# Optimization experiments

Hardware: AMD Instinct MI355X
Metric: run time of the kernel (lower is better)

The kernel has to match this reference:

```python
import jax, jax.numpy as jnp
import numpy as np

D_MODEL = 1024
D_HEAD = 128
BATCH = 4
SEQ = 4096


def setup_inputs() -> dict:
    key = jax.random.key(0)
    ks = jax.random.split(key, 7)
    s = 1.0 / np.sqrt(D_MODEL)
    return {
        "x": jax.random.normal(ks[0], (BATCH, SEQ, D_MODEL), dtype=jnp.float32),
        "Wq": jax.random.normal(ks[1], (D_MODEL, D_HEAD), dtype=jnp.float32) * s,
        "bq": jax.random.normal(ks[2], (D_HEAD,), dtype=jnp.float32) * 0.02,
        "Wk": jax.random.normal(ks[3], (D_MODEL, D_HEAD), dtype=jnp.float32) * s,
        "bk": jax.random.normal(ks[4], (D_HEAD,), dtype=jnp.float32) * 0.02,
        "Wv": jax.random.normal(ks[5], (D_MODEL, D_HEAD), dtype=jnp.float32) * s,
        "bv": jax.random.normal(ks[6], (D_HEAD,), dtype=jnp.float32) * 0.02,
    }


def reference(x, Wq, bq, Wk, bk, Wv, bv):
    # Single-head causal self-attention (intended math of MaskedAttention).
    # x: [B, S, D_MODEL]; projections to [B, S, D_HEAD].
    q = x @ Wq + bq
    k = x @ Wk + bk
    v = x @ Wv + bv
    scale = 1.0 / jnp.sqrt(jnp.asarray(D_HEAD, dtype=x.dtype))
    scores = jnp.einsum("bsd,btd->bst", q, k) * scale  # [B, S, S]
    # additive causal mask: -inf strictly above the diagonal
    s_len = scores.shape[-1]
    causal = jnp.tril(jnp.ones((s_len, s_len), dtype=bool))
    scores = jnp.where(causal[None, :, :], scores, jnp.asarray(-jnp.inf, dtype=scores.dtype))
    attn = jax.nn.softmax(scores, axis=-1)
    return jnp.einsum("bst,btd->bsd", attn, v)  # [B, S, D_HEAD]
```

## Files before the change

kernel.cpp:

```cpp
#include <hip/hip_runtime.h>
#include <stdint.h>
#include <stddef.h>

#define SEQ 4096
#define DM 1024
#define DH 128
#define NB 4
#define SPLITS 4

typedef __attribute__((ext_vector_type(8))) short bf16x8;
typedef __attribute__((ext_vector_type(4))) float f32x4;

__device__ __forceinline__ unsigned short f2bf(float f) {
    union { float f; uint32_t u; } v; v.f = f;
    uint32_t u = v.u + 0x7FFF + ((v.u >> 16) & 1);
    return (unsigned short)(u >> 16);
}

__device__ __forceinline__ uint32_t cvt_pk_bf16(float lo, float hi) {
    uint32_t r;
    asm("v_cvt_pk_bf16_f32 %0, %1, %2" : "=v"(r) : "v"(lo), "v"(hi));
    return r;
}

__device__ __forceinline__ void gload_lds16(const void* g, void* l) {
    __builtin_amdgcn_global_load_lds(
        (const __attribute__((address_space(1))) void*)g,
        (__attribute__((address_space(3))) void*)l, 16, 0, 0);
}

__global__ __launch_bounds__(256) void prep_kernel(
    const float* __restrict__ Wq, const float* __restrict__ Wk,
    const float* __restrict__ Wv, unsigned short* __restrict__ Wt)
{
    int idx = blockIdx.x * 256 + threadIdx.x;
    int n = idx >> 10, k = idx & 1023;
    int p = n >> 7, c = n & 127;
    const float* W = (p == 0) ? Wq : (p == 1) ? Wk : Wv;
    float v = W[k * DH + c];
    if (p == 0) v *= 0.08838834764831845f;
    Wt[idx] = f2bf(v);
}

__global__ __launch_bounds__(512) void proj_kernel(
    const float* __restrict__ x,
    const unsigned short* __restrict__ Wt,
    const float* __restrict__ bq, const float* __restrict__ bk,
    const float* __restrict__ bv,
    unsigned short* __restrict__ qb, unsigned short* __restrict__ kb,
    unsigned short* __restrict__ vt)
{
    __shared__ unsigned short A_lds[2][64 * 72];
    __shared__ unsigned short B_lds[2][384 * 64];
    const int tid = threadIdx.x;
    const int lane = tid & 63, w = tid >> 6;
    const int wm = w >> 2, wn = w & 3;
    const int q15 = lane & 15, g = lane >> 4;
    const int mt = blockIdx.x;

    const int arow = tid >> 3, aseg = tid & 7;

    f32x4 acc[2][6];
    #pragma unroll
    for (int mi = 0; mi < 2; ++mi)
        #pragma unroll
        for (int ni = 0; ni < 6; ++ni) acc[mi][ni] = (f32x4){0.f, 0.f, 0.f, 0.f};

    const float* asrc = x + (size_t)(mt * 64 + arow) * DM + aseg * 8;

    #pragma unroll
    for (int t = 0; t < 6; ++t) {
        int brow = t * 64 + arow;
        int bl = aseg ^ (brow & 7);
        gload_lds16(Wt + (size_t)brow * DM + bl * 8,
                    (char*)&B_lds[0][0] + t * 8192 + tid * 16);
    }
    {
        f32x4 lo4 = *(const f32x4*)asrc;
        f32x4 hi4 = *(const f32x4*)(asrc + 4);
        uint32_t* ad = (uint32_t*)&A_lds[0][arow * 72 + aseg * 8];
        ad[0] = cvt_pk_bf16(lo4[0], lo4[1]);
        ad[1] = cvt_pk_bf16(lo4[2], lo4[3]);
        ad[2] = cvt_pk_bf16(hi4[0], hi4[1]);
        ad[3] = cvt_pk_bf16(hi4[2], hi4[3]);
    }
    __syncthreads();

    int cur = 0;
    for (int kt = 0; kt < 16; ++kt) {
        f32x4 nlo, nhi;
        if (kt < 15) {
            #pragma unroll
            for (int t = 0; t < 6; ++t) {
                int brow = t * 64 + arow;
                int bl = aseg ^ (brow & 7);
                gload_lds16(Wt + (size_t)brow * DM + (kt + 1) * 64 + bl * 8,
                            (char*)&B_lds[cur ^ 1][0] + t * 8192 + tid * 16);
            }
            nlo = *(const f32x4*)(asrc + (kt + 1) * 64);
            nhi = *(const f32x4*)(asrc + (kt + 1) * 64 + 4);
        }
        #pragma unroll
        for (int kk = 0; kk < 2; ++kk) {
            bf16x8 af[2], bfr[6];
            #pragma unroll
            for (int mi = 0; mi < 2; ++mi)
                af[mi] = *(const bf16x8*)&A_lds[cur][(wm * 32 + mi * 16 + q15) * 72 + (kk * 4 + g) * 8];
            #pragma unroll
            for (int ni = 0; ni < 6; ++ni)
                bfr[ni] = *(const bf16x8*)&B_lds[cur][(wn * 96 + ni * 16 + q15) * 64 + ((kk * 4 + g) ^ (q15 & 7)) * 8];
            #pragma unroll
            for (int mi = 0; mi < 2; ++mi)
                #pragma unroll
                for (int ni = 0; ni < 6; ++ni)
                    acc[mi][ni] = __builtin_amdgcn_mfma_f32_16x16x32_bf16(
                        af[mi], bfr[ni], acc[mi][ni], 0, 0, 0);
        }
        if (kt < 15) {
            uint32_t* ad = (uint32_t*)&A_lds[cur ^ 1][arow * 72 + aseg * 8];
            ad[0] = cvt_pk_bf16(nlo[0], nlo[1]);
            ad[1] = cvt_pk_bf16(nlo[2], nlo[3]);
            ad[2] = cvt_pk_bf16(nhi[0], nhi[1]);
            ad[3] = cvt_pk_bf16(nhi[2], nhi[3]);
        }
        __syncthreads();
        cur ^= 1;
    }

    #pragma unroll
    for (int ni = 0; ni < 6; ++ni) {
        int n = wn * 96 + ni * 16 + q15;
        int p = n >> 7, c = n & 127;
        const float* bias = (p == 0) ? bq : (p == 1) ? bk : bv;
        float bval = bias[c] * ((p == 0) ? 0.08838834764831845f : 1.0f);
        #pragma unroll
        for (int mi = 0; mi < 2; ++mi) {
            int m0 = mt * 64 + wm * 32 + mi * 16 + g * 4;
            #pragma unroll
            for (int r = 0; r < 4; ++r) {
                unsigned short h = f2bf(acc[mi][ni][r] + bval);
                int m = m0 + r;
                if (p == 0) qb[(size_t)m * DH + c] = h;
                else if (p == 1) kb[(size_t)m * DH + c] = h;
                else vt[(size_t)((m >> 12) * 128 + c) * SEQ + (m & 4095)] = h;
            }
        }
    }
}

__global__ __launch_bounds__(512) void attn_kernel(
    const unsigned short* __restrict__ qb,
    const unsigned short* __restrict__ kb,
    const unsigned short* __restrict__ vt,
    float* __restrict__ po,
    float* __restrict__ pm, float* __restrict__ pl)
{
    __shared__ unsigned short K_lds[64 * 128];
    __shared__ unsigned short V_lds[128 * 64];
    __shared__ unsigned short P_lds[8 * 1024];
    const int tid = threadIdx.x;
    const int w = tid >> 6;
    const int lane = tid & 63;
    const int q15 = lane & 15, g = lane >> 4;
    const int xcd = blockIdx.x & 7, slot = blockIdx.x >> 3;
    const int b = xcd >> 1;
    const int j = 31 - (slot >> 1);
    const int s = (slot & 1) * 2 + (xcd & 1);
    const int n = 2 * j + 2;
    const int lo = (n * s) >> 2, hi = (n * (s + 1)) >> 2;
    if (lo >= hi) return;
    const int qbase = j * 128;
    const int wq0 = qbase + w * 16;
    const int qglob = wq0 + q15;

    bf16x8 qf[4];
    const unsigned short* qrow = qb + (size_t)(b * SEQ + qglob) * DH;
    #pragma unroll
    for (int kk = 0; kk < 4; ++kk) qf[kk] = *(const bf16x8*)(qrow + kk * 32 + g * 8);

    f32x4 o[8];
    #pragma unroll
    for (int f = 0; f < 8; ++f) o[f] = (f32x4){0.f, 0.f, 0.f, 0.f};
    float m_run = -60.0f, l_run = 0.f;

    const unsigned short* Kb = kb + (size_t)b * SEQ * DH;
    const unsigned short* Vb = vt + (size_t)b * 128 * SEQ;
    unsigned short* Pw = &P_lds[w * 1024];

    for (int kt = lo; kt < hi; ++kt) {
        {
            const unsigned short* Ksrc = Kb + (size_t)kt * 64 * DH;
            const unsigned short* Vsrc = Vb + kt * 64;
            #pragma unroll
            for (int i = 0; i < 2; ++i) {
                int krow = i * 32 + w * 4 + (lane >> 4);
                int kseg = (lane & 15) ^ (krow & 7);
                gload_lds16(Ksrc + (size_t)krow * DH + kseg * 8,
                            (char*)K_lds + i * 8192 + w * 1024);
                int vrow = i * 64 + w * 8 + (lane >> 3);
                int vseg = (lane & 7) ^ (vrow & 7);
                gload_lds16(Vsrc + (size_t)vrow * SEQ + vseg * 8,
                            (char*)V_lds + i * 8192 + w * 1024);
            }
        }
        __syncthreads();
        f32x4 sf[4];
        __builtin_amdgcn_s_setprio(1);
        #pragma unroll
        for (int mt2 = 0; mt2 < 4; ++mt2) {
            f32x4 sa = (f32x4){0.f, 0.f, 0.f, 0.f};
            #pragma unroll
            for (int kk = 0; kk < 4; ++kk) {
                int seg = (kk * 4 + g) ^ (q15 & 7);
                bf16x8 kf = *(const bf16x8*)&K_lds[(mt2 * 16 + q15) * 128 + seg * 8];
                sa = __builtin_amdgcn_mfma_f32_16x16x32_bf16(kf, qf[kk], sa, 0, 0, 0);
            }
            sf[mt2] = sa;
        }
        __builtin_amdgcn_s_setprio(0);
        float tmax = -__builtin_inff();
        if (kt * 64 + 63 > wq0) {
            #pragma unroll
            for (int mt2 = 0; mt2 < 4; ++mt2)
                #pragma unroll
                for (int r = 0; r < 4; ++r) {
                    int kglob = kt * 64 + mt2 * 16 + g * 4 + r;
                    float v = (kglob <= qglob) ? sf[mt2][r] : -__builtin_inff();
                    sf[mt2][r] = v;
                    tmax = fmaxf(tmax, v);
                }
        } else {
            #pragma unroll
            for (int mt2 = 0; mt2 < 4; ++mt2)
                #pragma unroll
                for (int r = 0; r < 4; ++r) tmax = fmaxf(tmax, sf[mt2][r]);
        }
        tmax = fmaxf(tmax, __shfl_xor(tmax, 16));
        tmax = fmaxf(tmax, __shfl_xor(tmax, 32));
        if (!__all((tmax - m_run) <= 8.0f)) {
            float m_new = fmaxf(m_run, tmax);
            float c = __expf(m_run - m_new);
            float cr[4];
            #pragma unroll
            for (int r = 0; r < 4; ++r) cr[r] = __shfl(c, g * 4 + r);
            #pragma unroll
            for (int f = 0; f < 8; ++f)
                #pragma unroll
                for (int r = 0; r < 4; ++r) o[f][r] *= cr[r];
            l_run *= c;
            m_run = m_new;
        }
        float rsum = 0.f;
        #pragma unroll
        for (int mt2 = 0; mt2 < 4; ++mt2)
            #pragma unroll
            for (int r = 0; r < 4; ++r) {
                float p = __expf(sf[mt2][r] - m_run);
                sf[mt2][r] = p;
                rsum += p;
            }
        rsum += __shfl_xor(rsum, 16);
        rsum += __shfl_xor(rsum, 32);
        l_run += rsum;
        #pragma unroll
        for (int mt2 = 0; mt2 < 4; ++mt2) {
            uint32_t p01 = cvt_pk_bf16(sf[mt2][0], sf[mt2][1]);
            uint32_t p23 = cvt_pk_bf16(sf[mt2][2], sf[mt2][3]);
            uint32_t* pd = (uint32_t*)(Pw + ((mt2 * 2 + (g >> 1)) * 16 + q15) * 8 + (g & 1) * 4);
            pd[0] = p01;
            pd[1] = p23;
        }
        asm volatile("s_waitcnt lgkmcnt(0)" ::: "memory");
        bf16x8 pf[2];
        #pragma unroll
        for (int kk2 = 0; kk2 < 2; ++kk2)
            pf[kk2] = *(const bf16x8*)&Pw[((kk2 * 4 + g) * 16 + q15) * 8];
        __builtin_amdgcn_s_setprio(1);
        #pragma unroll
        for (int f = 0; f < 8; ++f) {
            #pragma unroll
            for (int kk2 = 0; kk2 < 2; ++kk2) {
                int seg = (kk2 * 4 + g) ^ (q15 & 7);
                bf16x8 vf = *(const bf16x8*)&V_lds[(f * 16 + q15) * 64 + seg * 8];
                o[f] = __builtin_amdgcn_mfma_f32_16x16x32_bf16(pf[kk2], vf, o[f], 0, 0, 0);
            }
        }
        __builtin_amdgcn_s_setprio(0);
        __syncthreads();
    }
    float* pob = po + ((size_t)(s * NB + b) * SEQ + wq0) * DH;
    #pragma unroll
    for (int f = 0; f < 8; ++f)
        #pragma unroll
        for (int r = 0; r < 4; ++r)
            pob[(size_t)(g * 4 + r) * DH + f * 16 + q15] = o[f][r];
    if (g == 0) {
        size_t sidx = (size_t)(s * NB + b) * SEQ + wq0 + q15;
        pm[sidx] = m_run;
        pl[sidx] = l_run;
    }
}

__global__ __launch_bounds__(256) void reduce_kernel(
    const float* __restrict__ po, const float* __restrict__ pm,
    const float* __restrict__ pl, float* __restrict__ out)
{
    int r = blockIdx.x * 8 + (threadIdx.x >> 5);
    int d0 = (threadIdx.x & 31) * 4;
    int b = r >> 12, q = r & 4095;
    int n = 2 * (q >> 7) + 2;
    float ms[SPLITS];
    float M = -__builtin_inff();
    #pragma unroll
    for (int s = 0; s < SPLITS; ++s) {
        int lo = (n * s) >> 2, hi = (n * (s + 1)) >> 2;
        if (hi > lo) {
            ms[s] = pm[(size_t)(s * NB + b) * SEQ + q];
            M = fmaxf(M, ms[s]);
        } else ms[s] = -__builtin_inff();
    }
    float L = 0.f;
    f32x4 acc = (f32x4){0.f, 0.f, 0.f, 0.f};
    #pragma unroll
    for (int s = 0; s < SPLITS; ++s) {
        int lo = (n * s) >> 2, hi = (n * (s + 1)) >> 2;
        if (hi > lo) {
            float wgt = __expf(ms[s] - M);
            L += wgt * pl[(size_t)(s * NB + b) * SEQ + q];
            f32x4 p = *(const f32x4*)&po[((size_t)(s * NB + b) * SEQ + q) * DH + d0];
            acc += wgt * p;
        }
    }
    float inv = 1.0f / L;
    *(f32x4*)&out[((size_t)(b * SEQ) + q) * DH + d0] = acc * inv;
}

extern "C" void kernel_launch(void* const* d_in, const int* in_sizes, int n_in,
                              void* d_out, int out_size, void* d_ws, size_t ws_size,
                              hipStream_t stream)
{
    const float* x  = (const float*)d_in[0];
    const float* Wq = (const float*)d_in[1];
    const float* bq = (const float*)d_in[2];
    const float* Wk = (const float*)d_in[3];
    const float* bk = (const float*)d_in[4];
    const float* Wv = (const float*)d_in[5];
    const float* bv = (const float*)d_in[6];

    char* ws = (char*)d_ws;
    unsigned short* Wt = (unsigned short*)(ws + 33554432);
    unsigned short* qb = (unsigned short*)(ws + 34340864);
    unsigned short* kb = (unsigned short*)(ws + 38535168);
    unsigned short* vt = (unsigned short*)(ws + 42729472);
    float* po = (float*)(ws);
    float* pm = (float*)(ws + 33554432);
    float* pl = (float*)(ws + 33554432 + 262144);

    prep_kernel<<<1536, 256, 0, stream>>>(Wq, Wk, Wv, Wt);
    proj_kernel<<<256, 512, 0, stream>>>(x, Wt, bq, bk, bv, qb, kb, vt);
    attn_kernel<<<512, 512, 0, stream>>>(qb, kb, vt, po, pm, pl);
    reduce_kernel<<<2048, 256, 0, stream>>>(po, pm, pl, (float*)d_out);
}
```

Before: 175.1 us.

## Double-buffer K/V tiles in attention and split projection N across two blocks

The attention kernel now double-buffers K and V tiles in LDS, prefetching the next tile while computing on the current one, which removes the load-then-barrier stall each iteration. The projection kernel splits the 384-wide output across two blocks, doubling the grid to 512 blocks and halving per-block LDS and accumulators. It also reorders the softmax row-sum to come after the P stores. The cost is more LDS in attention (possible occupancy drop) and each x tile being converted twice in projection.

```diff
diff --git a/kernel.cpp b/kernel.cpp
--- a/kernel.cpp
+++ b/kernel.cpp
@@ -51,28 +51,31 @@
     unsigned short* __restrict__ vt)
 {
     __shared__ unsigned short A_lds[2][64 * 72];
-    __shared__ unsigned short B_lds[2][384 * 64];
+    __shared__ unsigned short B_lds[2][192 * 64];
     const int tid = threadIdx.x;
     const int lane = tid & 63, w = tid >> 6;
     const int wm = w >> 2, wn = w & 3;
     const int q15 = lane & 15, g = lane >> 4;
-    const int mt = blockIdx.x;
+    const int mt = blockIdx.x >> 1;
+    const int nt = blockIdx.x & 1;
+    const int nbase = nt * 192;
 
     const int arow = tid >> 3, aseg = tid & 7;
 
-    f32x4 acc[2][6];
+    f32x4 acc[2][3];
     #pragma unroll
     for (int mi = 0; mi < 2; ++mi)
         #pragma unroll
-        for (int ni = 0; ni < 6; ++ni) acc[mi][ni] = (f32x4){0.f, 0.f, 0.f, 0.f};
+        for (int ni = 0; ni < 3; ++ni) acc[mi][ni] = (f32x4){0.f, 0.f, 0.f, 0.f};
 
     const float* asrc = x + (size_t)(mt * 64 + arow) * DM + aseg * 8;
-
-    #pragma unroll
-    for (int t = 0; t < 6; ++t) {
+    const unsigned short* bsrc = Wt + (size_t)nbase * DM;
+
+    #pragma unroll
+    for (int t = 0; t < 3; ++t) {
         int brow = t * 64 + arow;
         int bl = aseg ^ (brow & 7);
-        gload_lds16(Wt + (size_t)brow * DM + bl * 8,
+        gload_lds16(bsrc + (size_t)brow * DM + bl * 8,
                     (char*)&B_lds[0][0] + t * 8192 + tid * 16);
     }
     {
@@ -91,10 +94,10 @@
         f32x4 nlo, nhi;
         if (kt < 15) {
             #pragma unroll
-            for (int t = 0; t < 6; ++t) {
+            for (int t = 0; t < 3; ++t) {
                 int brow = t * 64 + arow;
                 int bl = aseg ^ (brow & 7);
-                gload_lds16(Wt + (size_t)brow * DM + (kt + 1) * 64 + bl * 8,
+                gload_lds16(bsrc + (size_t)brow * DM + (kt + 1) * 64 + bl * 8,
                             (char*)&B_lds[cur ^ 1][0] + t * 8192 + tid * 16);
             }
             nlo = *(const f32x4*)(asrc + (kt + 1) * 64);
@@ -102,17 +105,17 @@
         }
         #pragma unroll
         for (int kk = 0; kk < 2; ++kk) {
-            bf16x8 af[2], bfr[6];
+            bf16x8 af[2], bfr[3];
             #pragma unroll
             for (int mi = 0; mi < 2; ++mi)
                 af[mi] = *(const bf16x8*)&A_lds[cur][(wm * 32 + mi * 16 + q15) * 72 + (kk * 4 + g) * 8];
             #pragma unroll
-            for (int ni = 0; ni < 6; ++ni)
-                bfr[ni] = *(const bf16x8*)&B_lds[cur][(wn * 96 + ni * 16 + q15) * 64 + ((kk * 4 + g) ^ (q15 & 7)) * 8];
+            for (int ni = 0; ni < 3; ++ni)
+                bfr[ni] = *(const bf16x8*)&B_lds[cur][(wn * 48 + ni * 16 + q15) * 64 + ((kk * 4 + g) ^ (q15 & 7)) * 8];
             #pragma unroll
             for (int mi = 0; mi < 2; ++mi)
                 #pragma unroll
-                for (int ni = 0; ni < 6; ++ni)
+                for (int ni = 0; ni < 3; ++ni)
                     acc[mi][ni] = __builtin_amdgcn_mfma_f32_16x16x32_bf16(
                         af[mi], bfr[ni], acc[mi][ni], 0, 0, 0);
         }
@@ -128,8 +131,8 @@
     }
 
     #pragma unroll
-    for (int ni = 0; ni < 6; ++ni) {
-        int n = wn * 96 + ni * 16 + q15;
+    for (int ni = 0; ni < 3; ++ni) {
+        int n = nbase + wn * 48 + ni * 16 + q15;
         int p = n >> 7, c = n & 127;
         const float* bias = (p == 0) ? bq : (p == 1) ? bk : bv;
         float bval = bias[c] * ((p == 0) ? 0.08838834764831845f : 1.0f);
@@ -155,8 +158,8 @@
     float* __restrict__ po,
     float* __restrict__ pm, float* __restrict__ pl)
 {
-    __shared__ unsigned short K_lds[64 * 128];
-    __shared__ unsigned short V_lds[128 * 64];
+    __shared__ unsigned short K_lds[2][64 * 128];
+    __shared__ unsigned short V_lds[2][128 * 64];
     __shared__ unsigned short P_lds[8 * 1024];
     const int tid = threadIdx.x;
     const int w = tid >> 6;
@@ -187,23 +190,43 @@
     const unsigned short* Vb = vt + (size_t)b * 128 * SEQ;
     unsigned short* Pw = &P_lds[w * 1024];
 
+    const int krow0 = w * 4 + (lane >> 4);
+    const int vrow0 = w * 8 + (lane >> 3);
+
+    {
+        const unsigned short* Ksrc = Kb + (size_t)lo * 64 * DH;
+        const unsigned short* Vsrc = Vb + lo * 64;
+        #pragma unroll
+        for (int i = 0; i < 2; ++i) {
+            int krow = i * 32 + krow0;
+            int kseg = (lane & 15) ^ (krow & 7);
+            gload_lds16(Ksrc + (size_t)krow * DH + kseg * 8,
+                        (char*)&K_lds[0][0] + i * 8192 + w * 1024);
+            int vrow = i * 64 + vrow0;
+            int vseg = (lane & 7) ^ (vrow & 7);
+            gload_lds16(Vsrc + (size_t)vrow * SEQ + vseg * 8,
+                        (char*)&V_lds[0][0] + i * 8192 + w * 1024);
+        }
+    }
+    __syncthreads();
+
+    int cur = 0;
     for (int kt = lo; kt < hi; ++kt) {
-        {
-            const unsigned short* Ksrc = Kb + (size_t)kt * 64 * DH;
-            const unsigned short* Vsrc = Vb + kt * 64;
+        if (kt + 1 < hi) {
+            const unsigned short* Ksrc = Kb + (size_t)(kt + 1) * 64 * DH;
+            const unsigned short* Vsrc = Vb + (kt + 1) * 64;
             #pragma unroll
             for (int i = 0; i < 2; ++i) {
-                int krow = i * 32 + w * 4 + (lane >> 4);
+                int krow = i * 32 + krow0;
                 int kseg = (lane & 15) ^ (krow & 7);
                 gload_lds16(Ksrc + (size_t)krow * DH + kseg * 8,
-                            (char*)K_lds + i * 8192 + w * 1024);
-                int vrow = i * 64 + w * 8 + (lane >> 3);
+                            (char*)&K_lds[cur ^ 1][0] + i * 8192 + w * 1024);
+                int vrow = i * 64 + vrow0;
                 int vseg = (lane & 7) ^ (vrow & 7);
                 gload_lds16(Vsrc + (size_t)vrow * SEQ + vseg * 8,
-                            (char*)V_lds + i * 8192 + w * 1024);
-            }
-        }
-        __syncthreads();
+                            (char*)&V_lds[cur ^ 1][0] + i * 8192 + w * 1024);
+            }
+        }
         f32x4 sf[4];
         __builtin_amdgcn_s_setprio(1);
         #pragma unroll
@@ -212,7 +235,7 @@
             #pragma unroll
             for (int kk = 0; kk < 4; ++kk) {
                 int seg = (kk * 4 + g) ^ (q15 & 7);
-                bf16x8 kf = *(const bf16x8*)&K_lds[(mt2 * 16 + q15) * 128 + seg * 8];
+                bf16x8 kf = *(const bf16x8*)&K_lds[cur][(mt2 * 16 + q15) * 128 + seg * 8];
                 sa = __builtin_amdgcn_mfma_f32_16x16x32_bf16(kf, qf[kk], sa, 0, 0, 0);
             }
             sf[mt2] = sa;
@@ -250,18 +273,11 @@
             l_run *= c;
             m_run = m_new;
         }
-        float rsum = 0.f;
         #pragma unroll
         for (int mt2 = 0; mt2 < 4; ++mt2)
             #pragma unroll
-            for (int r = 0; r < 4; ++r) {
-                float p = __expf(sf[mt2][r] - m_run);
-                sf[mt2][r] = p;
-                rsum += p;
-            }
-        rsum += __shfl_xor(rsum, 16);
-        rsum += __shfl_xor(rsum, 32);
-        l_run += rsum;
+            for (int r = 0; r < 4; ++r)
+                sf[mt2][r] = __expf(sf[mt2][r] - m_run);
         #pragma unroll
         for (int mt2 = 0; mt2 < 4; ++mt2) {
             uint32_t p01 = cvt_pk_bf16(sf[mt2][0], sf[mt2][1]);
@@ -270,6 +286,14 @@
             pd[0] = p01;
             pd[1] = p23;
         }
+        float rsum = 0.f;
+        #pragma unroll
+        for (int mt2 = 0; mt2 < 4; ++mt2)
+            #pragma unroll
+            for (int r = 0; r < 4; ++r) rsum += sf[mt2][r];
+        rsum += __shfl_xor(rsum, 16);
+        rsum += __shfl_xor(rsum, 32);
+        l_run += rsum;
         asm volatile("s_waitcnt lgkmcnt(0)" ::: "memory");
         bf16x8 pf[2];
         #pragma unroll
@@ -281,12 +305,13 @@
             #pragma unroll
             for (int kk2 = 0; kk2 < 2; ++kk2) {
                 int seg = (kk2 * 4 + g) ^ (q15 & 7);
-                bf16x8 vf = *(const bf16x8*)&V_lds[(f * 16 + q15) * 64 + seg * 8];
+                bf16x8 vf = *(const bf16x8*)&V_lds[cur][(f * 16 + q15) * 64 + seg * 8];
                 o[f] = __builtin_amdgcn_mfma_f32_16x16x32_bf16(pf[kk2], vf, o[f], 0, 0, 0);
             }
         }
         __builtin_amdgcn_s_setprio(0);
         __syncthreads();
+        cur ^= 1;
     }
     float* pob = po + ((size_t)(s * NB + b) * SEQ + wq0) * DH;
     #pragma unroll
@@ -357,7 +382,7 @@
     float* pl = (float*)(ws + 33554432 + 262144);
 
     prep_kernel<<<1536, 256, 0, stream>>>(Wq, Wk, Wv, Wt);
-    proj_kernel<<<256, 512, 0, stream>>>(x, Wt, bq, bk, bv, qb, kb, vt);
+    proj_kernel<<<512, 512, 0, stream>>>(x, Wt, bq, bk, bv, qb, kb, vt);
     attn_kernel<<<512, 512, 0, stream>>>(qb, kb, vt, po, pm, pl);
     reduce_kernel<<<2048, 256, 0, stream>>>(po, pm, pl, (float*)d_out);
 }
```

Result: slower. 181.4 us (+3.6%).
